# Kernel tuning notes

Hardware: AMD Instinct MI355X
Metric: run time of the kernel (lower is better)

Reference implementation:

```python
import jax, jax.numpy as jnp
import numpy as np

B, N, D, H = 4, 2048, 256, 4
NT, ET = 5, 6
HEAD = D // H


def _linear_params(k, fan_in, fan_out):
    # torch nn.Linear default init: U(-1/sqrt(fan_in), 1/sqrt(fan_in)) for W and b
    bound = 1.0 / np.sqrt(fan_in)
    kw, kb = jax.random.split(k)
    W = jax.random.uniform(kw, (fan_in, fan_out), minval=-bound, maxval=bound, dtype=jnp.float32)
    b = jax.random.uniform(kb, (fan_out,), minval=-bound, maxval=bound, dtype=jnp.float32)
    return W, b


def setup_inputs() -> dict:
    key = jax.random.key(0)
    ks = jax.random.split(key, 10)
    Wq, bq = _linear_params(ks[0], D, D)
    Wk, bk = _linear_params(ks[1], D, D)
    Wv, bv = _linear_params(ks[2], D, D)
    Wo, bo = _linear_params(ks[3], D, D)
    return {
        "nodes": jax.random.normal(ks[4], (B, N, D), dtype=jnp.float32),
        "node_types": jax.random.randint(ks[5], (B, N), 0, NT, dtype=jnp.int32),
        "edge_types": jax.random.randint(ks[6], (B, N, N), 0, ET, dtype=jnp.int32),
        "adjacency": jax.random.randint(ks[7], (B, N, N), 0, 2).astype(jnp.float32),
        "node_type_embed": jax.random.normal(ks[8], (NT, D), dtype=jnp.float32),  # nn.Embedding ~ N(0,1)
        "edge_type_embed": jax.random.normal(ks[9], (ET, H), dtype=jnp.float32),
        "Wq": Wq, "bq": bq, "Wk": Wk, "bk": bk, "Wv": Wv, "bv": bv, "Wo": Wo, "bo": bo,
        "ln_g": jnp.ones((D,), jnp.float32),
        "ln_b": jnp.zeros((D,), jnp.float32),
    }


def reference(nodes, node_types, edge_types, adjacency, node_type_embed, edge_type_embed,
              Wq, bq, Wk, bk, Wv, bv, Wo, bo, ln_g, ln_b):
    # add node-type embeddings (residual below uses the typed nodes, as in the torch code)
    x = nodes + node_type_embed[node_types]                      # [B,N,D]

    def split_heads(t):
        return t.reshape(B, N, H, HEAD).transpose(0, 2, 1, 3)    # [B,H,N,HEAD]

    Q = split_heads(x @ Wq + bq)
    K = split_heads(x @ Wk + bk)
    V = split_heads(x @ Wv + bv)

    scores = jnp.einsum('bhnd,bhmd->bhnm', Q, K) / np.sqrt(HEAD).astype(np.float32)

    # edge-type bias: [B,N,N,H] -> [B,H,N,N]
    scores = scores + jnp.transpose(edge_type_embed[edge_types], (0, 3, 1, 2))

    # type-match soft mask: match -> +0.1, mismatch -> -0.05  (== tm*0.15 - 0.05)
    tm = (node_types[:, :, None] == node_types[:, None, :]).astype(jnp.float32)
    scores = scores + (tm * 0.15 - 0.05)[:, None]

    # adjacency hard mask
    scores = scores + ((1.0 - adjacency) * -1e9)[:, None]

    attn = jax.nn.softmax(scores, axis=-1)                        # [B,H,N,N]
    ctx = jnp.einsum('bhnm,bhmd->bhnd', attn, V)
    ctx = ctx.transpose(0, 2, 1, 3).reshape(B, N, D)

    out = ctx @ Wo + bo
    y = x + out
    mu = jnp.mean(y, axis=-1, keepdims=True)
    var = jnp.var(y, axis=-1, keepdims=True)
    y = (y - mu) * jax.lax.rsqrt(var + 1e-5) * ln_g + ln_b
    return y, attn
```

## Files before the change

### kernel.cpp

```cpp
#include <hip/hip_runtime.h>

#define Bsz 4
#define Nn 2048
#define Dd 256
#define Hh 4
#define HD 64
#define NTt 5
#define ETt 6
#define LOG2E 1.4426950408889634f
#define MSUB 24.0f
#define SCLQ 0.18033688011112042f

typedef float f32x4 __attribute__((ext_vector_type(4)));
typedef __bf16 bf16x8 __attribute__((ext_vector_type(8)));
typedef unsigned int u32x4 __attribute__((ext_vector_type(4)));
typedef unsigned short u16;
typedef unsigned char u8;
typedef unsigned int uint;

static __device__ __forceinline__ u16 f2bf(float f) {
  unsigned int u = __builtin_bit_cast(unsigned int, f);
  u = (u + 0x7fffu + ((u >> 16) & 1u)) >> 16;
  return (u16)u;
}

static __device__ __forceinline__ bf16x8 ld8(const u16* p) {
  return __builtin_bit_cast(bf16x8, *(const u32x4*)p);
}

static __device__ __forceinline__ void stage16(const void* g, void* l) {
  __builtin_amdgcn_global_load_lds(
      (const __attribute__((address_space(1))) uint*)g,
      (__attribute__((address_space(3))) uint*)l, 16, 0, 0);
}

#define MFMA16(a, b, c) __builtin_amdgcn_mfma_f32_16x16x32_bf16((a), (b), (c), 0, 0, 0)

#define OFF_X      0u
#define OFF_XBF    8388608u
#define OFF_WQKVT  12582912u
#define OFF_WOT    12976128u
#define OFF_BQKV   13107200u
#define OFF_Q      13110272u
#define OFF_K      17304576u
#define OFF_VT     25693184u
#define OFF_CTX    29887488u
#define OFF_CODES  34081792u

__global__ void pack_kernel(const float* Wq, const float* Wk, const float* Wv,
                            const float* Wo, const float* bq, const float* bk,
                            const float* bv, u16* wqkvT, u16* woT, float* bqkv) {
  int tid = blockIdx.x * 256 + threadIdx.x;
  if (tid < 196608) {
    int c = tid >> 8, k = tid & 255;
    int which = c >> 8, cc = c & 255;
    const float* W = (which == 0) ? Wq : ((which == 1) ? Wk : Wv);
    wqkvT[tid] = f2bf(W[k * 256 + cc]);
  } else if (tid < 262144) {
    int t2 = tid - 196608;
    int c = t2 >> 8, k = t2 & 255;
    woT[t2] = f2bf(Wo[k * 256 + c]);
  } else if (tid < 262912) {
    int c = tid - 262144;
    int which = c >> 8, cc = c & 255;
    bqkv[c] = (which == 0) ? bq[cc] : ((which == 1) ? bk[cc] : bv[cc]);
  }
}

__global__ void embed_kernel(const float* nodes, const int* node_types,
                             const float* nte, float* xf, u16* xbf) {
  int t = blockIdx.x * 256 + threadIdx.x;
  int flat = t * 4;
  int bn = flat >> 8, d0 = flat & 255;
  int nt = node_types[bn];
  float4 nv = *(const float4*)(nodes + flat);
  float4 ev = *(const float4*)(nte + nt * 256 + d0);
  float4 x4;
  x4.x = nv.x + ev.x; x4.y = nv.y + ev.y; x4.z = nv.z + ev.z; x4.w = nv.w + ev.w;
  *(float4*)(xf + flat) = x4;
  ushort4 xb;
  xb.x = f2bf(x4.x); xb.y = f2bf(x4.y); xb.z = f2bf(x4.z); xb.w = f2bf(x4.w);
  *(ushort4*)(xbf + flat) = xb;
}

__global__ __launch_bounds__(256) void maskpack_kernel(
    const int* node_types, const int* edge_types, const float* adjacency,
    u8* codes) {
  __shared__ uint lw[16 * 516 + 4];
  int blk = blockIdx.x;
  int qt = blk & 127;
  int b = blk >> 7;
  int t = threadIdx.x;
  const int* ntb = node_types + b * Nn;
  const int* etb = edge_types + (size_t)b * Nn * Nn + (size_t)qt * 16 * Nn;
  const float* adjb = adjacency + (size_t)b * Nn * Nn + (size_t)qt * 16 * Nn;

#pragma unroll 4
  for (int a = 0; a < 32; ++a) {
    int idx = a * 256 + t;
    int row = idx >> 9;
    int k4 = idx & 511;
    int k0 = k4 * 4;
    int ntq = ntb[qt * 16 + row];
    int4 et4 = *(const int4*)(etb + (size_t)row * Nn + k0);
    float4 a4 = *(const float4*)(adjb + (size_t)row * Nn + k0);
    int4 nt4 = *(const int4*)(ntb + k0);
    int e[4] = {et4.x, et4.y, et4.z, et4.w};
    int n[4] = {nt4.x, nt4.y, nt4.z, nt4.w};
    float av[4] = {a4.x, a4.y, a4.z, a4.w};
    uint word = 0;
#pragma unroll
    for (int j = 0; j < 4; ++j) {
      int code = e[j] + ((ntq == n[j]) ? 6 : 0) + ((av[j] != 0.0f) ? 12 : 0);
      word |= (uint)(code * 4) << (8 * j);
    }
    lw[row * 516 + k4] = word;
  }
  __syncthreads();

  u8* rec = codes + (size_t)(b * 128 + qt) * 32768;
#pragma unroll
  for (int c = 0; c < 8; ++c) {
    int W = (c * 256 + t) * 4;
    int kt = W >> 8;
    int rem = W & 255;
    int l4 = rem >> 6;
    int l15 = (rem >> 2) & 15;
    int base = l15 * 516 + kt * 16 + l4;
    u32x4 o = {lw[base], lw[base + 4], lw[base + 8], lw[base + 12]};
    *(u32x4*)(rec + (size_t)W * 4) = o;
  }
}

__global__ __launch_bounds__(256) void qkv_kernel(const u16* xbf, const u16* wqkvT,
                                                  const float* bqkv,
                                                  u16* Qb, u16* Kb, u16* Vtb) {
  int cb = blockIdx.x;
  int rb = blockIdx.y;
  int w = threadIdx.x >> 6, lane = threadIdx.x & 63;
  int l15 = lane & 15, l4 = lane >> 4;
  int row0 = rb * 64 + w * 16;
  int col0 = cb * 64;
  const u16* xr = xbf + (size_t)(row0 + l15) * 256;
  f32x4 acc[4];
#pragma unroll
  for (int i = 0; i < 4; ++i) acc[i] = (f32x4){0.f, 0.f, 0.f, 0.f};
#pragma unroll
  for (int kst = 0; kst < 8; ++kst) {
    int k0 = kst * 32 + l4 * 8;
    bf16x8 a = ld8(xr + k0);
#pragma unroll
    for (int cs = 0; cs < 4; ++cs) {
      int col = col0 + cs * 16 + l15;
      bf16x8 bw = ld8(wqkvT + (size_t)col * 256 + k0);
      acc[cs] = MFMA16(a, bw, acc[cs]);
    }
  }
#pragma unroll
  for (int cs = 0; cs < 4; ++cs) {
    int col = col0 + cs * 16 + l15;
    float bias = bqkv[col];
    int which = col >> 8, c = col & 255;
    int h = c >> 6, hd = c & 63;
    float scale = (which == 0) ? SCLQ : 1.0f;
#pragma unroll
    for (int j = 0; j < 4; ++j) {
      int row = row0 + l4 * 4 + j;
      int bb = row >> 11, n = row & 2047;
      u16 val = f2bf((acc[cs][j] + bias) * scale);
      if (which == 2)
        Vtb[((size_t)((bb * Hh + h) * HD + hd)) * Nn + n] = val;
      else if (which == 0)
        Qb[(size_t)(((bb * Hh + h) * Nn + n)) * HD + hd] = val;
      else
        Kb[(size_t)(((bb * Hh + h) * Nn + n)) * HD + hd] = val;
    }
  }
}

__global__ __launch_bounds__(256) void attn_kernel(
    const u16* Qb, const u16* Kb, const u16* Vtb, const u8* codes,
    const float* ee_g, float* attn_out, u16* ctx_ws) {
  __shared__ __align__(16) char kvb[4][2][8192];
  __shared__ __align__(16) char pls[4][2048];
  __shared__ float lsh[4][16];

  int bid0 = blockIdx.x;
  int bid = ((bid0 & 7) << 8) | (bid0 >> 3);
  int qt = bid & 127;
  int h = (bid >> 7) & 3;
  int b = bid >> 9;
  int w = threadIdx.x >> 6, lane = threadIdx.x & 63;
  int l15 = lane & 15, l4 = lane >> 4;
  int q0 = qt * 16;
  int bh = b * Hh + h;
  int wk0 = w * 512;

  float lutv = 0.f;
  {
    int ln = lane;
    int et = ln - 6 * (ln / 6);
    int tm = (ln / 6) & 1;
    int adj = ln / 12;
    if (ln < 24)
      lutv = (ee_g[et * Hh + h] + (tm ? 0.10f : -0.05f)) * LOG2E +
             (adj ? 0.f : -1.442695041e9f) - MSUB;
  }
  int lut_i = __float_as_int(lutv);

  const u16* Qp = Qb + (size_t)(bh * Nn + q0 + l15) * HD;
  bf16x8 bq0 = ld8(Qp + l4 * 8);
  bf16x8 bq1 = ld8(Qp + 32 + l4 * 8);

  const char* Kgw = (const char*)(Kb + (size_t)bh * Nn * HD) + (size_t)wk0 * 128;
  const char* Vg = (const char*)(Vtb + (size_t)bh * HD * Nn);
  const u32x4* cp = (const u32x4*)codes + ((size_t)(b * 128 + qt) * 32) * 64;

  int oS[8];
  const char* KgS[8];
  const char* VgS[8];
#pragma unroll
  for (int j = 0; j < 8; ++j) {
    int o = j * 1024 + lane * 16;
    oS[j] = o;
    int row = o >> 7;
    int sz = (o ^ ((row & 7) << 4)) & 127;
    KgS[j] = Kgw + (size_t)row * 128 + sz;
    VgS[j] = Vg + (size_t)row * (Nn * 2) + wk0 * 2 + sz;
  }
  char* myb0 = (char*)kvb[w][0];
  char* myb1 = (char*)kvb[w][1];

  int sw = (l15 & 7) << 4;
  int ra = (l15 * 128 + l4 * 16) ^ sw;
  char* pwave = (char*)pls[w];
  int pwbase = l15 * 128;

  uint p[8][8];
  float accl = 0.f;

#pragma unroll
  for (int j = 0; j < 8; ++j) stage16(KgS[j], myb0 + oS[j]);
  u32x4 cw = cp[(size_t)(w * 8) * 64 + lane];

#pragma unroll
  for (int i = 0; i < 8; ++i) {
    u32x4 cwn = cw;
    if (i < 7) {
      char* nb = (i & 1) ? myb0 : myb1;
#pragma unroll
      for (int j = 0; j < 8; ++j)
        stage16(KgS[j] + (size_t)(i + 1) * 8192, nb + oS[j]);
      cwn = cp[(size_t)(w * 8 + i + 1) * 64 + lane];
    }
    __builtin_amdgcn_sched_barrier(0);
    if (i < 7) asm volatile("s_waitcnt vmcnt(9) lgkmcnt(0)" ::: "memory");
    else       asm volatile("s_waitcnt vmcnt(0) lgkmcnt(0)" ::: "memory");
    __builtin_amdgcn_sched_barrier(0);
    const char* kcur = (i & 1) ? myb1 : myb0;
#pragma unroll
    for (int ks = 0; ks < 4; ++ks) {
      unsigned int cword = cw[ks];
      f32x4 acc;
#pragma unroll
      for (int j = 0; j < 4; ++j)
        acc[j] = __int_as_float(
            __builtin_amdgcn_ds_bpermute((cword >> (8 * j)) & 0xFF, lut_i));
      acc = MFMA16(ld8((const u16*)(kcur + ra + ks * 2048)), bq0, acc);
      acc = MFMA16(ld8((const u16*)(kcur + (ra ^ 64) + ks * 2048)), bq1, acc);
      float e0 = __builtin_amdgcn_exp2f(acc[0]);
      float e1 = __builtin_amdgcn_exp2f(acc[1]);
      float e2 = __builtin_amdgcn_exp2f(acc[2]);
      float e3 = __builtin_amdgcn_exp2f(acc[3]);
      accl += (e0 + e1) + (e2 + e3);
      asm("v_cvt_pk_bf16_f32 %0, %1, %2" : "=v"(p[i][ks * 2]) : "v"(e0), "v"(e1));
      asm("v_cvt_pk_bf16_f32 %0, %1, %2" : "=v"(p[i][ks * 2 + 1]) : "v"(e2), "v"(e3));
    }
    cw = cwn;
  }
  accl += __shfl_xor(accl, 16);
  accl += __shfl_xor(accl, 32);
  if (lane < 16) lsh[w][lane] = accl;
  __syncthreads();
  float tot = lsh[0][l15] + lsh[1][l15] + lsh[2][l15] + lsh[3][l15];
  bool zrow = (tot == 0.0f);
  float cscale = zrow ? (1.0f / 2048.0f) : (1.0f / tot);

  f32x4 ctx[4];
#pragma unroll
  for (int i = 0; i < 4; ++i) ctx[i] = (f32x4){0.f, 0.f, 0.f, 0.f};
  float* attb = attn_out + (size_t)bh * Nn * Nn + (size_t)(q0 + l15) * Nn + wk0;

#pragma unroll
  for (int j = 0; j < 8; ++j) stage16(VgS[j], myb0 + oS[j]);

#pragma unroll
  for (int i = 0; i < 8; ++i) {
    if (i < 7) {
      char* nb = (i & 1) ? myb0 : myb1;
#pragma unroll
      for (int j = 0; j < 8; ++j)
        stage16(VgS[j] + (size_t)(i + 1) * 128, nb + oS[j]);
    }
    __builtin_amdgcn_sched_barrier(0);
    if (i == 0)     asm volatile("s_waitcnt vmcnt(8) lgkmcnt(0)" ::: "memory");
    else if (i < 7) asm volatile("s_waitcnt vmcnt(12) lgkmcnt(0)" ::: "memory");
    else            asm volatile("s_waitcnt vmcnt(4) lgkmcnt(0)" ::: "memory");
    __builtin_amdgcn_sched_barrier(0);
    const char* vcur = (i & 1) ? myb1 : myb0;

    uint pp[8];
#pragma unroll
    for (int r = 0; r < 8; ++r) pp[r] = zrow ? 0x3F803F80u : p[i][r];
#pragma unroll
    for (int ks = 0; ks < 4; ++ks) {
      int2 wv = {(int)pp[ks * 2], (int)pp[ks * 2 + 1]};
      *(int2*)(pwave + pwbase + ((ks * 32 + l4 * 8) ^ sw)) = wv;
    }
#pragma unroll
    for (int ks = 0; ks < 4; ++ks) {
      uint u0 = pp[ks * 2], u1 = pp[ks * 2 + 1];
      f32x4 o;
      o[0] = __int_as_float((int)(u0 << 16)) * cscale;
      o[1] = __int_as_float((int)(u0 & 0xFFFF0000u)) * cscale;
      o[2] = __int_as_float((int)(u1 << 16)) * cscale;
      o[3] = __int_as_float((int)(u1 & 0xFFFF0000u)) * cscale;
      __builtin_nontemporal_store(o, (f32x4*)(attb + i * 64 + ks * 16 + l4 * 4));
    }
#pragma unroll
    for (int half = 0; half < 2; ++half) {
      bf16x8 pa = ld8((const u16*)(pwave + pwbase + ((half * 64 + l4 * 16) ^ sw)));
#pragma unroll
      for (int d = 0; d < 4; ++d) {
        bf16x8 v = ld8((const u16*)(vcur + d * 2048 + l15 * 128 +
                                    ((half * 64 + l4 * 16) ^ sw)));
        ctx[d] = MFMA16(pa, v, ctx[d]);
      }
    }
  }

  float csr[4];
#pragma unroll
  for (int j = 0; j < 4; ++j)
    csr[j] = __int_as_float(
        __builtin_amdgcn_ds_bpermute((l4 * 4 + j) * 4, __float_as_int(cscale)));
#pragma unroll
  for (int d = 0; d < 4; ++d)
#pragma unroll
    for (int j = 0; j < 4; ++j) ctx[d][j] *= csr[j];

  __syncthreads();
  float* creg = (float*)kvb;
  if (w > 0) {
    float* cs_ = creg + ((size_t)(w - 1) * 64 + lane) * 17;
#pragma unroll
    for (int d = 0; d < 4; ++d)
#pragma unroll
      for (int j = 0; j < 4; ++j) cs_[d * 4 + j] = ctx[d][j];
  }
  __syncthreads();
  if (w == 0) {
    float* c0 = creg + (size_t)lane * 17;
    float* c1 = creg + ((size_t)64 + lane) * 17;
    float* c2 = creg + ((size_t)128 + lane) * 17;
#pragma unroll
    for (int d = 0; d < 4; ++d) {
      int col = h * 64 + d * 16 + l15;
#pragma unroll
      for (int j = 0; j < 4; ++j) {
        float v = ctx[d][j] + c0[d * 4 + j] + c1[d * 4 + j] + c2[d * 4 + j];
        int qrow = q0 + l4 * 4 + j;
        ctx_ws[(size_t)(b * Nn + qrow) * Dd + col] = f2bf(v);
      }
    }
  }
}

__global__ __launch_bounds__(256) void outln_kernel(const u16* ctxb, const u16* woT,
                                                    const float* bo, const float* xf,
                                                    const float* ln_g, const float* ln_b,
                                                    float* yout) {
  __shared__ float ytile[32][257];
  __shared__ float muS[32], rvS[32];
  int bm0 = blockIdx.x * 32;
  int w = threadIdx.x >> 6, lane = threadIdx.x & 63;
  int l15 = lane & 15, l4 = lane >> 4;
  f32x4 acc[2][4];
#pragma unroll
  for (int q = 0; q < 2; ++q)
#pragma unroll
    for (int i = 0; i < 4; ++i) acc[q][i] = (f32x4){0.f, 0.f, 0.f, 0.f};
#pragma unroll
  for (int kst = 0; kst < 8; ++kst) {
    int k0 = kst * 32 + l4 * 8;
    bf16x8 a0 = ld8(ctxb + (size_t)(bm0 + l15) * 256 + k0);
    bf16x8 a1 = ld8(ctxb + (size_t)(bm0 + 16 + l15) * 256 + k0);
#pragma unroll
    for (int ds_ = 0; ds_ < 4; ++ds_) {
      bf16x8 bw = ld8(woT + (size_t)(w * 64 + ds_ * 16 + l15) * 256 + k0);
      acc[0][ds_] = MFMA16(a0, bw, acc[0][ds_]);
      acc[1][ds_] = MFMA16(a1, bw, acc[1][ds_]);
    }
  }
#pragma unroll
  for (int qs = 0; qs < 2; ++qs)
#pragma unroll
    for (int ds_ = 0; ds_ < 4; ++ds_) {
      int col = w * 64 + ds_ * 16 + l15;
      float bof = bo[col];
#pragma unroll
      for (int j = 0; j < 4; ++j) {
        int row = qs * 16 + l4 * 4 + j;
        ytile[row][col] = acc[qs][ds_][j] + bof + xf[(size_t)(bm0 + row) * 256 + col];
      }
    }
  __syncthreads();
  int row = threadIdx.x >> 3, seg = threadIdx.x & 7;
  float ps = 0.f, pq = 0.f;
#pragma unroll
  for (int c = 0; c < 32; ++c) {
    float v = ytile[row][seg * 32 + c];
    ps += v; pq += v * v;
  }
  ps += __shfl_xor(ps, 1); pq += __shfl_xor(pq, 1);
  ps += __shfl_xor(ps, 2); pq += __shfl_xor(pq, 2);
  ps += __shfl_xor(ps, 4); pq += __shfl_xor(pq, 4);
  if (seg == 0) {
    float mu = ps * (1.0f / 256.0f);
    muS[row] = mu;
    rvS[row] = rsqrtf(pq * (1.0f / 256.0f) - mu * mu + 1e-5f);
  }
  __syncthreads();
  float mu = muS[row], rv = rvS[row];
  float* yr = yout + (size_t)(bm0 + row) * 256;
#pragma unroll
  for (int c0 = 0; c0 < 32; c0 += 4) {
    int c = seg * 32 + c0;
    float4 o;
    o.x = (ytile[row][c + 0] - mu) * rv * ln_g[c + 0] + ln_b[c + 0];
    o.y = (ytile[row][c + 1] - mu) * rv * ln_g[c + 1] + ln_b[c + 1];
    o.z = (ytile[row][c + 2] - mu) * rv * ln_g[c + 2] + ln_b[c + 2];
    o.w = (ytile[row][c + 3] - mu) * rv * ln_g[c + 3] + ln_b[c + 3];
    *(float4*)(yr + c) = o;
  }
}

extern "C" void kernel_launch(void* const* d_in, const int* in_sizes, int n_in,
                              void* d_out, int out_size, void* d_ws, size_t ws_size,
                              hipStream_t stream) {
  const float* nodes = (const float*)d_in[0];
  const int* node_types = (const int*)d_in[1];
  const int* edge_types = (const int*)d_in[2];
  const float* adjacency = (const float*)d_in[3];
  const float* nte = (const float*)d_in[4];
  const float* ee = (const float*)d_in[5];
  const float* Wq = (const float*)d_in[6];
  const float* bq = (const float*)d_in[7];
  const float* Wk = (const float*)d_in[8];
  const float* bk = (const float*)d_in[9];
  const float* Wv = (const float*)d_in[10];
  const float* bv = (const float*)d_in[11];
  const float* Wo = (const float*)d_in[12];
  const float* bo = (const float*)d_in[13];
  const float* ln_g = (const float*)d_in[14];
  const float* ln_b = (const float*)d_in[15];

  float* y = (float*)d_out;
  float* attn = y + (size_t)Bsz * Nn * Dd;

  char* ws = (char*)d_ws;
  float* xf = (float*)(ws + OFF_X);
  u16* xbf = (u16*)(ws + OFF_XBF);
  u16* wqkvT = (u16*)(ws + OFF_WQKVT);
  u16* woT = (u16*)(ws + OFF_WOT);
  float* bqkv = (float*)(ws + OFF_BQKV);
  u16* Qb = (u16*)(ws + OFF_Q);
  u16* Kb = (u16*)(ws + OFF_K);
  u16* Vtb = (u16*)(ws + OFF_VT);
  u16* ctxb = (u16*)(ws + OFF_CTX);
  u8* codes = (u8*)(ws + OFF_CODES);

  pack_kernel<<<1027, 256, 0, stream>>>(Wq, Wk, Wv, Wo, bq, bk, bv, wqkvT, woT, bqkv);
  embed_kernel<<<2048, 256, 0, stream>>>(nodes, node_types, nte, xf, xbf);
  maskpack_kernel<<<512, 256, 0, stream>>>(node_types, edge_types, adjacency, codes);
  qkv_kernel<<<dim3(12, 128), 256, 0, stream>>>(xbf, wqkvT, bqkv, Qb, Kb, Vtb);
  attn_kernel<<<2048, 256, 0, stream>>>(Qb, Kb, Vtb, codes, ee, attn, ctxb);
  outln_kernel<<<256, 256, 0, stream>>>(ctxb, woT, bo, xf, ln_g, ln_b, y);
}
```

Baseline: 184.5 us.

## Split attention key range across eight waves per block instead of four

```diff
diff --git a/kernel.cpp b/kernel.cpp
--- a/kernel.cpp
+++ b/kernel.cpp
@@ -14,6 +14,7 @@
 typedef float f32x4 __attribute__((ext_vector_type(4)));
 typedef __bf16 bf16x8 __attribute__((ext_vector_type(8)));
 typedef unsigned int u32x4 __attribute__((ext_vector_type(4)));
+typedef unsigned int u32x2 __attribute__((ext_vector_type(2)));
 typedef unsigned short u16;
 typedef unsigned char u8;
 typedef unsigned int uint;
@@ -178,12 +179,10 @@
   }
 }
 
-__global__ __launch_bounds__(256) void attn_kernel(
+__global__ __launch_bounds__(512, 4) void attn_kernel(
     const u16* Qb, const u16* Kb, const u16* Vtb, const u8* codes,
     const float* ee_g, float* attn_out, u16* ctx_ws) {
-  __shared__ __align__(16) char kvb[4][2][8192];
-  __shared__ __align__(16) char pls[4][2048];
-  __shared__ float lsh[4][16];
+  __shared__ __align__(16) char smem[81920];
 
   int bid0 = blockIdx.x;
   int bid = ((bid0 & 7) << 8) | (bid0 >> 3);
@@ -194,7 +193,12 @@
   int l15 = lane & 15, l4 = lane >> 4;
   int q0 = qt * 16;
   int bh = b * Hh + h;
-  int wk0 = w * 512;
+  int wk0 = w * 256;
+
+  float* lsh = (float*)(smem + 65536);
+  char* pwave = smem + 65536 + w * 2048;
+  char* kv0 = smem + w * 8192;
+  char* kv1 = kv0 + 4096;
 
   float lutv = 0.f;
   {
@@ -212,62 +216,62 @@
   bf16x8 bq0 = ld8(Qp + l4 * 8);
   bf16x8 bq1 = ld8(Qp + 32 + l4 * 8);
 
-  const char* Kgw = (const char*)(Kb + (size_t)bh * Nn * HD) + (size_t)wk0 * 128;
-  const char* Vg = (const char*)(Vtb + (size_t)bh * HD * Nn);
-  const u32x4* cp = (const u32x4*)codes + ((size_t)(b * 128 + qt) * 32) * 64;
-
-  int oS[8];
-  const char* KgS[8];
-  const char* VgS[8];
-#pragma unroll
-  for (int j = 0; j < 8; ++j) {
-    int o = j * 1024 + lane * 16;
-    oS[j] = o;
-    int row = o >> 7;
-    int sz = (o ^ ((row & 7) << 4)) & 127;
-    KgS[j] = Kgw + (size_t)row * 128 + sz;
-    VgS[j] = Vg + (size_t)row * (Nn * 2) + wk0 * 2 + sz;
-  }
-  char* myb0 = (char*)kvb[w][0];
-  char* myb1 = (char*)kvb[w][1];
-
-  int sw = (l15 & 7) << 4;
-  int ra = (l15 * 128 + l4 * 16) ^ sw;
-  char* pwave = (char*)pls[w];
-  int pwbase = l15 * 128;
-
-  uint p[8][8];
+  const char* Kg = (const char*)Kb + (size_t)bh * Nn * 128 + (size_t)wk0 * 128;
+  const char* KgS[4];
+  {
+    int colK = ((lane & 7) * 16) ^ (((lane >> 3) & 7) << 4);
+#pragma unroll
+    for (int j = 0; j < 4; ++j)
+      KgS[j] = Kg + (size_t)(j * 8 + (lane >> 3)) * 128 + colK;
+  }
+  const char* Vg = (const char*)Vtb + (size_t)bh * HD * Nn * 2 + (size_t)wk0 * 2;
+  const char* VgS[4];
+  {
+    int sV = (((lane & 3) ^ (lane >> 4)) & 3) * 16;
+#pragma unroll
+    for (int j = 0; j < 4; ++j)
+      VgS[j] = Vg + (size_t)(j * 16 + (lane >> 2)) * (Nn * 2) + sV;
+  }
+
+  const char* cpb = (const char*)codes + (size_t)(b * 128 + qt) * 32768 +
+                    (size_t)(w * 4) * 1024 + lane * 16;
+
+  int swK = (l15 & 7) << 4;
+  int raK = (l15 * 128 + l4 * 16) ^ swK;
+  int rv = l15 * 64 + ((l4 ^ ((l15 >> 2) & 3)) * 16);
+
+  uint p[8][4];
   float accl = 0.f;
 
-#pragma unroll
-  for (int j = 0; j < 8; ++j) stage16(KgS[j], myb0 + oS[j]);
-  u32x4 cw = cp[(size_t)(w * 8) * 64 + lane];
+  u32x2 cw = *(const u32x2*)cpb;
+#pragma unroll
+  for (int j = 0; j < 4; ++j) stage16(KgS[j], kv0 + j * 1024);
 
 #pragma unroll
   for (int i = 0; i < 8; ++i) {
-    u32x4 cwn = cw;
+    u32x2 cwn = cw;
+    char* kcur = (i & 1) ? kv1 : kv0;
+    char* knxt = (i & 1) ? kv0 : kv1;
     if (i < 7) {
-      char* nb = (i & 1) ? myb0 : myb1;
-#pragma unroll
-      for (int j = 0; j < 8; ++j)
-        stage16(KgS[j] + (size_t)(i + 1) * 8192, nb + oS[j]);
-      cwn = cp[(size_t)(w * 8 + i + 1) * 64 + lane];
+      cwn = *(const u32x2*)(cpb + ((i + 1) >> 1) * 1024 + ((i + 1) & 1) * 8);
+#pragma unroll
+      for (int j = 0; j < 4; ++j)
+        stage16(KgS[j] + (size_t)(i + 1) * 4096, knxt + j * 1024);
     }
     __builtin_amdgcn_sched_barrier(0);
-    if (i < 7) asm volatile("s_waitcnt vmcnt(9) lgkmcnt(0)" ::: "memory");
+    if (i < 7) asm volatile("s_waitcnt vmcnt(5) lgkmcnt(0)" ::: "memory");
     else       asm volatile("s_waitcnt vmcnt(0) lgkmcnt(0)" ::: "memory");
     __builtin_amdgcn_sched_barrier(0);
-    const char* kcur = (i & 1) ? myb1 : myb0;
-#pragma unroll
-    for (int ks = 0; ks < 4; ++ks) {
-      unsigned int cword = cw[ks];
+#pragma unroll
+    for (int ks = 0; ks < 2; ++ks) {
+      uint cword = cw[ks];
       f32x4 acc;
 #pragma unroll
       for (int j = 0; j < 4; ++j)
         acc[j] = __int_as_float(
-            __builtin_amdgcn_ds_bpermute((cword >> (8 * j)) & 0xFF, lut_i));
-      acc = MFMA16(ld8((const u16*)(kcur + ra + ks * 2048)), bq0, acc);
-      acc = MFMA16(ld8((const u16*)(kcur + (ra ^ 64) + ks * 2048)), bq1, acc);
+            __builtin_amdgcn_ds_bpermute((int)((cword >> (8 * j)) & 0xFFu), lut_i));
+      acc = MFMA16(ld8((const u16*)(kcur + raK + ks * 2048)), bq0, acc);
+      acc = MFMA16(ld8((const u16*)(kcur + (raK ^ 64) + ks * 2048)), bq1, acc);
       float e0 = __builtin_amdgcn_exp2f(acc[0]);
       float e1 = __builtin_amdgcn_exp2f(acc[1]);
       float e2 = __builtin_amdgcn_exp2f(acc[2]);
@@ -280,11 +284,14 @@
   }
   accl += __shfl_xor(accl, 16);
   accl += __shfl_xor(accl, 32);
-  if (lane < 16) lsh[w][lane] = accl;
-  __syncthreads();
-  float tot = lsh[0][l15] + lsh[1][l15] + lsh[2][l15] + lsh[3][l15];
+  if (lane < 16) lsh[w * 16 + lane] = accl;
+  __syncthreads();
+  float tot = 0.f;
+#pragma unroll
+  for (int ww = 0; ww < 8; ++ww) tot += lsh[ww * 16 + l15];
   bool zrow = (tot == 0.0f);
   float cscale = zrow ? (1.0f / 2048.0f) : (1.0f / tot);
+  __syncthreads();
 
   f32x4 ctx[4];
 #pragma unroll
@@ -292,50 +299,47 @@
   float* attb = attn_out + (size_t)bh * Nn * Nn + (size_t)(q0 + l15) * Nn + wk0;
 
 #pragma unroll
-  for (int j = 0; j < 8; ++j) stage16(VgS[j], myb0 + oS[j]);
+  for (int j = 0; j < 4; ++j) stage16(VgS[j], kv0 + j * 1024);
 
 #pragma unroll
   for (int i = 0; i < 8; ++i) {
+    char* vcur = (i & 1) ? kv1 : kv0;
+    char* vnxt = (i & 1) ? kv0 : kv1;
     if (i < 7) {
-      char* nb = (i & 1) ? myb0 : myb1;
-#pragma unroll
-      for (int j = 0; j < 8; ++j)
-        stage16(VgS[j] + (size_t)(i + 1) * 128, nb + oS[j]);
+#pragma unroll
+      for (int j = 0; j < 4; ++j)
+        stage16(VgS[j] + (size_t)(i + 1) * 64, vnxt + j * 1024);
     }
     __builtin_amdgcn_sched_barrier(0);
-    if (i == 0)     asm volatile("s_waitcnt vmcnt(8) lgkmcnt(0)" ::: "memory");
-    else if (i < 7) asm volatile("s_waitcnt vmcnt(12) lgkmcnt(0)" ::: "memory");
-    else            asm volatile("s_waitcnt vmcnt(4) lgkmcnt(0)" ::: "memory");
+    if (i == 0)     asm volatile("s_waitcnt vmcnt(4) lgkmcnt(0)" ::: "memory");
+    else if (i < 7) asm volatile("s_waitcnt vmcnt(6) lgkmcnt(0)" ::: "memory");
+    else            asm volatile("s_waitcnt vmcnt(2) lgkmcnt(0)" ::: "memory");
     __builtin_amdgcn_sched_barrier(0);
-    const char* vcur = (i & 1) ? myb1 : myb0;
-
-    uint pp[8];
-#pragma unroll
-    for (int r = 0; r < 8; ++r) pp[r] = zrow ? 0x3F803F80u : p[i][r];
-#pragma unroll
-    for (int ks = 0; ks < 4; ++ks) {
+
+    uint pp[4];
+#pragma unroll
+    for (int r = 0; r < 4; ++r) pp[r] = zrow ? 0x3F803F80u : p[i][r];
+#pragma unroll
+    for (int ks = 0; ks < 2; ++ks) {
+      int slot = (ks * 2 + (l4 >> 1)) ^ ((l15 >> 2) & 3);
       int2 wv = {(int)pp[ks * 2], (int)pp[ks * 2 + 1]};
-      *(int2*)(pwave + pwbase + ((ks * 32 + l4 * 8) ^ sw)) = wv;
-    }
-#pragma unroll
-    for (int ks = 0; ks < 4; ++ks) {
+      *(int2*)(pwave + l15 * 64 + slot * 16 + (l4 & 1) * 8) = wv;
+    }
+#pragma unroll
+    for (int ks = 0; ks < 2; ++ks) {
       uint u0 = pp[ks * 2], u1 = pp[ks * 2 + 1];
       f32x4 o;
       o[0] = __int_as_float((int)(u0 << 16)) * cscale;
       o[1] = __int_as_float((int)(u0 & 0xFFFF0000u)) * cscale;
       o[2] = __int_as_float((int)(u1 << 16)) * cscale;
       o[3] = __int_as_float((int)(u1 & 0xFFFF0000u)) * cscale;
-      __builtin_nontemporal_store(o, (f32x4*)(attb + i * 64 + ks * 16 + l4 * 4));
-    }
-#pragma unroll
-    for (int half = 0; half < 2; ++half) {
-      bf16x8 pa = ld8((const u16*)(pwave + pwbase + ((half * 64 + l4 * 16) ^ sw)));
-#pragma unroll
-      for (int d = 0; d < 4; ++d) {
-        bf16x8 v = ld8((const u16*)(vcur + d * 2048 + l15 * 128 +
-                                    ((half * 64 + l4 * 16) ^ sw)));
-        ctx[d] = MFMA16(pa, v, ctx[d]);
-      }
+      __builtin_nontemporal_store(o, (f32x4*)(attb + i * 32 + ks * 16 + l4 * 4));
+    }
+    bf16x8 pa = ld8((const u16*)(pwave + rv));
+#pragma unroll
+    for (int d = 0; d < 4; ++d) {
+      bf16x8 v = ld8((const u16*)(vcur + d * 1024 + rv));
+      ctx[d] = MFMA16(pa, v, ctx[d]);
     }
   }
 
@@ -350,7 +354,7 @@
     for (int j = 0; j < 4; ++j) ctx[d][j] *= csr[j];
 
   __syncthreads();
-  float* creg = (float*)kvb;
+  float* creg = (float*)smem;
   if (w > 0) {
     float* cs_ = creg + ((size_t)(w - 1) * 64 + lane) * 17;
 #pragma unroll
@@ -360,15 +364,15 @@
   }
   __syncthreads();
   if (w == 0) {
-    float* c0 = creg + (size_t)lane * 17;
-    float* c1 = creg + ((size_t)64 + lane) * 17;
-    float* c2 = creg + ((size_t)128 + lane) * 17;
 #pragma unroll
     for (int d = 0; d < 4; ++d) {
       int col = h * 64 + d * 16 + l15;
 #pragma unroll
       for (int j = 0; j < 4; ++j) {
-        float v = ctx[d][j] + c0[d * 4 + j] + c1[d * 4 + j] + c2[d * 4 + j];
+        float v = ctx[d][j];
+#pragma unroll
+        for (int ww = 0; ww < 7; ++ww)
+          v += creg[((size_t)ww * 64 + lane) * 17 + d * 4 + j];
         int qrow = q0 + l4 * 4 + j;
         ctx_ws[(size_t)(b * Nn + qrow) * Dd + col] = f2bf(v);
       }
@@ -484,6 +488,6 @@
   embed_kernel<<<2048, 256, 0, stream>>>(nodes, node_types, nte, xf, xbf);
   maskpack_kernel<<<512, 256, 0, stream>>>(node_types, edge_types, adjacency, codes);
   qkv_kernel<<<dim3(12, 128), 256, 0, stream>>>(xbf, wqkvT, bqkv, Qb, Kb, Vtb);
-  attn_kernel<<<2048, 256, 0, stream>>>(Qb, Kb, Vtb, codes, ee, attn, ctxb);
+  attn_kernel<<<2048, 512, 0, stream>>>(Qb, Kb, Vtb, codes, ee, attn, ctxb);
   outln_kernel<<<256, 256, 0, stream>>>(ctxb, woT, bo, xf, ln_g, ln_b, y);
 }
```

Result: faster. 179.6 us (-2.6%).
